# Kernel optimization log

Measured on AMD Instinct MI355X. Metric: run time of the kernel, lower is better.

The kernel has to match this reference:

```python
import jax, jax.numpy as jnp
import numpy as np

EMBED_DIM = 1024
FFN_DIM = 4096
N_WIRES = 8
BATCH, SEQ = 16, 2048


def setup_inputs() -> dict:
    key = jax.random.key(0)
    ks = jax.random.split(key, 6)
    x = jax.random.normal(ks[0], (BATCH, SEQ, EMBED_DIM), dtype=jnp.float32)
    # trainable RY angles (torchquantum inits uniform in [0, 2*pi))
    theta = jax.random.uniform(ks[1], (N_WIRES,), dtype=jnp.float32) * 2.0 * jnp.pi
    # torch Linear params: W [out, in], b [out], kaiming-uniform-ish scale
    lim1 = 1.0 / np.sqrt(N_WIRES)
    W1 = jax.random.uniform(ks[2], (FFN_DIM, N_WIRES), minval=-lim1, maxval=lim1, dtype=jnp.float32)
    b1 = jax.random.uniform(ks[3], (FFN_DIM,), minval=-lim1, maxval=lim1, dtype=jnp.float32)
    lim2 = 1.0 / np.sqrt(FFN_DIM)
    W2 = jax.random.uniform(ks[4], (EMBED_DIM, FFN_DIM), minval=-lim2, maxval=lim2, dtype=jnp.float32)
    b2 = jax.random.uniform(ks[5], (EMBED_DIM,), minval=-lim2, maxval=lim2, dtype=jnp.float32)
    return {"x": x, "theta": theta, "W1": W1, "b1": b1, "W2": W2, "b2": b2}


def reference(x, theta, W1, b1, W2, b2):
    # Quantum circuit on n_wires=8 qubits: RX(x_i) encode on |0>, then RY(theta_i),
    # then <Z_i>. All gates are single-qubit on a product state, so exactly:
    #   <Z_i> = cos(x_i) * cos(theta_i)
    qz = jnp.cos(x[..., :N_WIRES]) * jnp.cos(theta)  # [B, S, 8]
    # dropout in eval mode = identity
    h = jax.nn.relu(jnp.einsum('bsw,fw->bsf', qz, W1) + b1)  # [B, S, ffn]
    out = jnp.einsum('bsf,ef->bse', h, W2) + b2  # [B, S, embed]
    return out
```

## Files before the change

### kernel.cpp

```cpp
#include <hip/hip_runtime.h>
#include <hip/hip_bf16.h>
#include <math.h>

#define EMBED 1024
#define FFN   4096
#define NW    8
#define MTOT  32768

#define BM 256
#define BN 256
#define BK 64
#define NT (FFN / BK)

#define STRIP 128
#define KPT   8

typedef __attribute__((ext_vector_type(8))) short          short8v;
typedef __attribute__((ext_vector_type(8))) unsigned short ushort8v;
typedef __attribute__((ext_vector_type(4))) float          f32x4;

typedef __attribute__((address_space(1))) void gvoid_t;
typedef __attribute__((address_space(3))) void svoid_t;

#define VMCNT(n)  asm volatile("s_waitcnt vmcnt(" #n ")" ::: "memory")
#define BAR()     __builtin_amdgcn_s_barrier()

static __device__ __forceinline__ unsigned short bf16bits(float f) {
    __hip_bfloat16 h = __float2bfloat16(f);
    return *reinterpret_cast<unsigned short*>(&h);
}

__global__ __launch_bounds__(256) void cvtW2_kernel(const float* __restrict__ W2,
                                                    __hip_bfloat16* __restrict__ Bw) {
    const long i0 = ((long)blockIdx.x * 256 + threadIdx.x) * 8;
    const float4 a = *(const float4*)(W2 + i0);
    const float4 b = *(const float4*)(W2 + i0 + 4);
    float fs[8] = {a.x, a.y, a.z, a.w, b.x, b.y, b.z, b.w};
    ushort8v v;
#pragma unroll
    for (int t = 0; t < 8; ++t) v[t] = bf16bits(fs[t]);
    *reinterpret_cast<ushort8v*>(Bw + i0) = v;
}

__global__ __launch_bounds__(256) void hprod2_kernel(
    const float* __restrict__ x, const float* __restrict__ theta,
    const float* __restrict__ W1, const float* __restrict__ b1,
    __hip_bfloat16* __restrict__ h, int m0)
{
    __shared__ float qz_lds[STRIP][NW];
    const int tid   = threadIdx.x;
    const int khalf = blockIdx.x & 1;
    const int strip = blockIdx.x >> 1;
    const int k0    = khalf * 2048 + tid * KPT;

    float w1r[KPT][NW];
    float b1r[KPT];
#pragma unroll
    for (int i = 0; i < KPT; ++i) {
        const float4 a = *(const float4*)(W1 + (long)(k0 + i) * NW);
        const float4 b = *(const float4*)(W1 + (long)(k0 + i) * NW + 4);
        w1r[i][0] = a.x; w1r[i][1] = a.y; w1r[i][2] = a.z; w1r[i][3] = a.w;
        w1r[i][4] = b.x; w1r[i][5] = b.y; w1r[i][6] = b.z; w1r[i][7] = b.w;
        b1r[i] = b1[k0 + i];
    }

    if (tid < STRIP) {
        const long m = (long)m0 + (long)strip * STRIP + tid;
        const float* xr = x + m * (long)EMBED;
#pragma unroll
        for (int w = 0; w < NW; ++w)
            qz_lds[tid][w] = cosf(xr[w]) * cosf(theta[w]);
    }
    __syncthreads();

    __hip_bfloat16* hp = h + ((long)strip * STRIP) * FFN + k0;
    for (int r = 0; r < STRIP; ++r) {
        float q[NW];
#pragma unroll
        for (int w = 0; w < NW; ++w) q[w] = qz_lds[r][w];
        ushort8v hv;
#pragma unroll
        for (int i = 0; i < KPT; ++i) {
            float acc = b1r[i];
#pragma unroll
            for (int w = 0; w < NW; ++w) acc = fmaf(q[w], w1r[i][w], acc);
            hv[i] = bf16bits(fmaxf(acc, 0.0f));
        }
        *reinterpret_cast<ushort8v*>(hp + (long)r * FFN) = hv;
    }
}

__global__ __launch_bounds__(512, 2) void gemm8_kernel(
    const __hip_bfloat16* __restrict__ A,
    const __hip_bfloat16* __restrict__ Bw,
    const float* __restrict__ b2,
    float* __restrict__ out, long m0, int nPm)
{
    __shared__ __align__(16) __hip_bfloat16 As[2][BM * BK];
    __shared__ __align__(16) __hip_bfloat16 Bs[2][BN * BK];

    const int tid = threadIdx.x, wid = tid >> 6, lane = tid & 63;
    const int l15 = lane & 15, l4 = lane >> 4;
    const int wr = wid >> 2, wc = wid & 3;

    const int xcd = blockIdx.x & 7, kb = blockIdx.x >> 3;
    const int pn  = kb & 3;
    const int pm  = xcd * (nPm >> 3) + (kb >> 2);

    const int srow  = tid >> 3;
    const int colsw = ((tid & 7) ^ (srow & 7)) * 8;

    const __hip_bfloat16* Ag = A  + (long)(pm * BM + srow) * FFN + colsw;
    const __hip_bfloat16* Bg = Bw + (long)(pn * BN + srow) * FFN + colsw;

    f32x4 acc[8][4];
#pragma unroll
    for (int i = 0; i < 8; ++i)
#pragma unroll
        for (int j = 0; j < 4; ++j) acc[i][j] = (f32x4){0.f, 0.f, 0.f, 0.f};

#define STAGE_A6(t, h) do {                                                     \
    __hip_bfloat16* _s = &As[(t) & 1][((h) * 128 + wid * 8) * BK];              \
    const __hip_bfloat16* _g = Ag + (long)((h) * 128) * FFN + (t) * BK;         \
    __builtin_amdgcn_global_load_lds((gvoid_t*)_g, (svoid_t*)_s, 16, 0, 0);     \
    __builtin_amdgcn_global_load_lds((gvoid_t*)(_g + (long)64 * FFN),           \
                                     (svoid_t*)(_s + 64 * BK), 16, 0, 0);       \
} while (0)

#define STAGE_B6(t, h) do {                                                     \
    __hip_bfloat16* _s = &Bs[(t) & 1][((h) * 128 + wid * 8) * BK];              \
    const __hip_bfloat16* _g = Bg + (long)((h) * 128) * FFN + (t) * BK;         \
    __builtin_amdgcn_global_load_lds((gvoid_t*)_g, (svoid_t*)_s, 16, 0, 0);     \
    __builtin_amdgcn_global_load_lds((gvoid_t*)(_g + (long)64 * FFN),           \
                                     (svoid_t*)(_s + 64 * BK), 16, 0, 0);       \
} while (0)

    const int rx = (l15 & 7) << 3;

    short8v aF[4][2];
    short8v bF[2][2][2];

#define READ_A6(t, a) do { _Pragma("unroll")                                    \
    for (int mi = 0; mi < 4; ++mi) {                                            \
        const int row = wr * 128 + (a) * 64 + mi * 16 + l15;                    \
        _Pragma("unroll") for (int kk = 0; kk < 2; ++kk)                        \
            aF[mi][kk] = *reinterpret_cast<const short8v*>(                     \
                &As[(t) & 1][row * BK + ((kk * 32 + l4 * 8) ^ rx)]);            \
    } } while (0)

#define READ_B6(t, b) do { _Pragma("unroll")                                    \
    for (int ni = 0; ni < 2; ++ni) {                                            \
        const int row = wc * 64 + (b) * 32 + ni * 16 + l15;                     \
        _Pragma("unroll") for (int kk = 0; kk < 2; ++kk)                        \
            bF[b][ni][kk] = *reinterpret_cast<const short8v*>(                  \
                &Bs[(t) & 1][row * BK + ((kk * 32 + l4 * 8) ^ rx)]);            \
    } } while (0)

#define MFMA_Q(aa, bb) do { _Pragma("unroll")                                   \
    for (int mi = 0; mi < 4; ++mi) _Pragma("unroll")                            \
    for (int ni = 0; ni < 2; ++ni) _Pragma("unroll")                            \
    for (int kk = 0; kk < 2; ++kk)                                              \
        acc[(aa) * 4 + mi][(bb) * 2 + ni] =                                     \
            __builtin_amdgcn_mfma_f32_16x16x32_bf16(                            \
                aF[mi][kk], bF[bb][ni][kk], acc[(aa) * 4 + mi][(bb) * 2 + ni],  \
                0, 0, 0);                                                       \
} while (0)

    STAGE_A6(0, 0); STAGE_A6(0, 1); STAGE_B6(0, 0); STAGE_B6(0, 1);
    STAGE_A6(1, 0);
    VMCNT(2); BAR();

    for (int t = 0; t < NT; ++t) {
        if (t + 1 < NT) STAGE_A6(t + 1, 1);
        READ_A6(t, 0); READ_B6(t, 0);
        BAR();
        __builtin_amdgcn_s_setprio(1); MFMA_Q(0, 0); __builtin_amdgcn_s_setprio(0);
        BAR();
        if (t + 1 < NT) STAGE_B6(t + 1, 0);
        READ_B6(t, 1);
        BAR();
        __builtin_amdgcn_s_setprio(1); MFMA_Q(0, 1); __builtin_amdgcn_s_setprio(0);
        BAR();
        if (t + 1 < NT) STAGE_B6(t + 1, 1);
        READ_A6(t, 1);
        BAR();
        __builtin_amdgcn_s_setprio(1); MFMA_Q(1, 1); __builtin_amdgcn_s_setprio(0);
        BAR();
        if (t + 2 < NT) STAGE_A6(t + 2, 0);
        BAR();
        __builtin_amdgcn_s_setprio(1); MFMA_Q(1, 0); __builtin_amdgcn_s_setprio(0);
        if (t < NT - 2) { VMCNT(2); } else { VMCNT(0); }
        BAR();
    }

#undef STAGE_A6
#undef STAGE_B6
#undef READ_A6
#undef READ_B6
#undef MFMA_Q

    const int gn0 = pn * BN + wc * 64;
    float bias[4];
#pragma unroll
    for (int ni = 0; ni < 4; ++ni) bias[ni] = b2[gn0 + ni * 16 + l15];
    const long gm0 = m0 + (long)pm * BM + wr * 128;
#pragma unroll
    for (int mi = 0; mi < 8; ++mi)
#pragma unroll
        for (int ni = 0; ni < 4; ++ni)
#pragma unroll
            for (int j = 0; j < 4; ++j) {
                const long row = gm0 + mi * 16 + l4 * 4 + j;
                out[row * EMBED + gn0 + ni * 16 + l15] = acc[mi][ni][j] + bias[ni];
            }
}

extern "C" void kernel_launch(void* const* d_in, const int* in_sizes, int n_in,
                              void* d_out, int out_size, void* d_ws, size_t ws_size,
                              hipStream_t stream)
{
    const float* x     = (const float*)d_in[0];
    const float* theta = (const float*)d_in[1];
    const float* W1    = (const float*)d_in[2];
    const float* b1    = (const float*)d_in[3];
    const float* W2    = (const float*)d_in[4];
    const float* b2    = (const float*)d_in[5];
    float* out = (float*)d_out;

    const size_t w2b = (size_t)EMBED * FFN * 2;
    __hip_bfloat16* Bw = (__hip_bfloat16*)d_ws;
    __hip_bfloat16* h  = (__hip_bfloat16*)((char*)d_ws + w2b);
    const size_t avail = ws_size > w2b ? ws_size - w2b : 0;

    long chunk = (long)((avail / ((size_t)FFN * 2)) & ~2047UL);
    if (chunk > MTOT) chunk = MTOT;
    if (chunk < 2048) chunk = 2048;

    cvtW2_kernel<<<(EMBED * FFN) / 2048, 256, 0, stream>>>(W2, Bw);

    for (long m0 = 0; m0 < MTOT; m0 += chunk) {
        const long rows = (MTOT - m0 < chunk) ? (MTOT - m0) : chunk;
        hprod2_kernel<<<(int)((rows / STRIP) * 2), 256, 0, stream>>>(
            x, theta, W1, b1, h, (int)m0);
        const int nPm = (int)(rows / BM);
        gemm8_kernel<<<nPm * 4, 512, 0, stream>>>(h, Bw, b2, out, m0, nPm);
    }
}
```

Before: 426.8 us.

## Reorder GEMM staging by quadrant and cap chunk size at half the rows

Rearranges how A and B tiles are staged into LDS so that each staged piece matches the quadrant consumed by the next MFMA phase. The prefetch of the next K-tile is spread across the four phases, with finer vmcnt waits in between. The row chunk is also capped at 16384, so the h producer and GEMM run as two smaller passes, which keeps the intermediate smaller and possibly more cache-resident at the cost of an extra launch pair. The new wait counts and schedule carry a risk of subtle ordering hazards.

```diff
diff --git a/kernel.cpp b/kernel.cpp
--- a/kernel.cpp
+++ b/kernel.cpp
@@ -90,7 +90,7 @@
     }
 }
 
-__global__ __launch_bounds__(512, 2) void gemm8_kernel(
+__global__ __launch_bounds__(512, 2) void gemm15_kernel(
     const __hip_bfloat16* __restrict__ A,
     const __hip_bfloat16* __restrict__ Bw,
     const float* __restrict__ b2,
@@ -109,9 +109,10 @@
 
     const int srow  = tid >> 3;
     const int colsw = ((tid & 7) ^ (srow & 7)) * 8;
+    const int brow  = ((wid >> 1) << 6) + ((wid & 1) << 3) + (lane >> 3);
 
     const __hip_bfloat16* Ag = A  + (long)(pm * BM + srow) * FFN + colsw;
-    const __hip_bfloat16* Bg = Bw + (long)(pn * BN + srow) * FFN + colsw;
+    const __hip_bfloat16* Bg = Bw + (long)(pn * BN + brow) * FFN + colsw;
 
     f32x4 acc[8][4];
 #pragma unroll
@@ -120,19 +121,20 @@
         for (int j = 0; j < 4; ++j) acc[i][j] = (f32x4){0.f, 0.f, 0.f, 0.f};
 
 #define STAGE_A6(t, h) do {                                                     \
-    __hip_bfloat16* _s = &As[(t) & 1][((h) * 128 + wid * 8) * BK];              \
-    const __hip_bfloat16* _g = Ag + (long)((h) * 128) * FFN + (t) * BK;         \
-    __builtin_amdgcn_global_load_lds((gvoid_t*)_g, (svoid_t*)_s, 16, 0, 0);     \
-    __builtin_amdgcn_global_load_lds((gvoid_t*)(_g + (long)64 * FFN),           \
-                                     (svoid_t*)(_s + 64 * BK), 16, 0, 0);       \
+    const __hip_bfloat16* _g = Ag + (long)((h) * 64) * FFN + (t) * BK;          \
+    __builtin_amdgcn_global_load_lds((gvoid_t*)_g,                              \
+        (svoid_t*)(&As[(t) & 1][((h) * 64 + wid * 8) * BK]), 16, 0, 0);         \
+    __builtin_amdgcn_global_load_lds((gvoid_t*)(_g + (long)128 * FFN),          \
+        (svoid_t*)(&As[(t) & 1][((h) * 64 + 128 + wid * 8) * BK]), 16, 0, 0);   \
 } while (0)
 
 #define STAGE_B6(t, h) do {                                                     \
-    __hip_bfloat16* _s = &Bs[(t) & 1][((h) * 128 + wid * 8) * BK];              \
-    const __hip_bfloat16* _g = Bg + (long)((h) * 128) * FFN + (t) * BK;         \
-    __builtin_amdgcn_global_load_lds((gvoid_t*)_g, (svoid_t*)_s, 16, 0, 0);     \
-    __builtin_amdgcn_global_load_lds((gvoid_t*)(_g + (long)64 * FFN),           \
-                                     (svoid_t*)(_s + 64 * BK), 16, 0, 0);       \
+    const __hip_bfloat16* _g = Bg + (long)((h) * 32) * FFN + (t) * BK;          \
+    const int _r = (h) * 32 + ((wid >> 1) << 6) + ((wid & 1) << 3);             \
+    __builtin_amdgcn_global_load_lds((gvoid_t*)_g,                              \
+        (svoid_t*)(&Bs[(t) & 1][_r * BK]), 16, 0, 0);                           \
+    __builtin_amdgcn_global_load_lds((gvoid_t*)(_g + (long)16 * FFN),           \
+        (svoid_t*)(&Bs[(t) & 1][(_r + 16) * BK]), 16, 0, 0);                    \
 } while (0)
 
     const int rx = (l15 & 7) << 3;
@@ -166,30 +168,31 @@
                 0, 0, 0);                                                       \
 } while (0)
 
-    STAGE_A6(0, 0); STAGE_A6(0, 1); STAGE_B6(0, 0); STAGE_B6(0, 1);
-    STAGE_A6(1, 0);
-    VMCNT(2); BAR();
+    STAGE_A6(0, 0); STAGE_B6(0, 0); STAGE_B6(0, 1); STAGE_A6(0, 1);
+    VMCNT(4); BAR();
 
     for (int t = 0; t < NT; ++t) {
-        if (t + 1 < NT) STAGE_A6(t + 1, 1);
         READ_A6(t, 0); READ_B6(t, 0);
         BAR();
         __builtin_amdgcn_s_setprio(1); MFMA_Q(0, 0); __builtin_amdgcn_s_setprio(0);
-        BAR();
-        if (t + 1 < NT) STAGE_B6(t + 1, 0);
+        VMCNT(2);
+        BAR();
+        if (t + 1 < NT) { STAGE_A6(t + 1, 0); STAGE_B6(t + 1, 0); }
         READ_B6(t, 1);
         BAR();
         __builtin_amdgcn_s_setprio(1); MFMA_Q(0, 1); __builtin_amdgcn_s_setprio(0);
+        if (t + 1 < NT) { VMCNT(4); }
+        else            { VMCNT(0); }
         BAR();
         if (t + 1 < NT) STAGE_B6(t + 1, 1);
         READ_A6(t, 1);
         BAR();
         __builtin_amdgcn_s_setprio(1); MFMA_Q(1, 1); __builtin_amdgcn_s_setprio(0);
         BAR();
-        if (t + 2 < NT) STAGE_A6(t + 2, 0);
+        if (t + 1 < NT) STAGE_A6(t + 1, 1);
         BAR();
         __builtin_amdgcn_s_setprio(1); MFMA_Q(1, 0); __builtin_amdgcn_s_setprio(0);
-        if (t < NT - 2) { VMCNT(2); } else { VMCNT(0); }
+        VMCNT(4);
         BAR();
     }
 
@@ -233,8 +236,8 @@
     const size_t avail = ws_size > w2b ? ws_size - w2b : 0;
 
     long chunk = (long)((avail / ((size_t)FFN * 2)) & ~2047UL);
-    if (chunk > MTOT) chunk = MTOT;
-    if (chunk < 2048) chunk = 2048;
+    if (chunk > 16384) chunk = 16384;
+    if (chunk < 2048)  chunk = 2048;
 
     cvtW2_kernel<<<(EMBED * FFN) / 2048, 256, 0, stream>>>(W2, Bw);
 
@@ -243,6 +246,6 @@
         hprod2_kernel<<<(int)((rows / STRIP) * 2), 256, 0, stream>>>(
             x, theta, W1, b1, h, (int)m0);
         const int nPm = (int)(rows / BM);
-        gemm8_kernel<<<nPm * 4, 512, 0, stream>>>(h, Bw, b2, out, m0, nPm);
-    }
-}
+        gemm15_kernel<<<nPm * 4, 512, 0, stream>>>(h, Bw, b2, out, m0, nPm);
+    }
+}
```

Result: faster. 386.8 us (-9.4%).
